# Performance work log

Hardware: AMD Instinct MI355X
Metric: run time of the kernel (lower is better)

Reference implementation:

```python
import jax, jax.numpy as jnp
import numpy as np

N = 50000          # nodes
E = 1600000        # edges
IN_C = 128
HID = 128
OUT_C = 1
NUM_LAYERS = 3     # extra conv2 applications
NUM_GRAPHS = 128


def setup_inputs() -> dict:
    key = jax.random.key(0)
    ks = jax.random.split(key, 10)
    x = jax.random.normal(ks[0], (N, IN_C), dtype=jnp.float32)
    edge_index = jax.random.randint(ks[1], (2, E), 0, N, dtype=jnp.int64)
    batch = jnp.sort(jax.random.randint(ks[2], (N,), 0, NUM_GRAPHS, dtype=jnp.int64))
    s1 = 1.0 / np.sqrt(IN_C)
    s2 = 1.0 / np.sqrt(HID)
    W1 = jax.random.uniform(ks[3], (IN_C, HID), jnp.float32, -s1, s1)
    b1 = jnp.zeros((HID,), jnp.float32)
    W2 = jax.random.uniform(ks[4], (HID, HID), jnp.float32, -s2, s2)
    b2 = jnp.zeros((HID,), jnp.float32)
    Wfc = jax.random.uniform(ks[5], (HID, OUT_C), jnp.float32, -s2, s2)
    bfc = jnp.zeros((OUT_C,), jnp.float32)
    return {"x": x, "edge_index": edge_index, "batch": batch,
            "W1": W1, "b1": b1, "W2": W2, "b2": b2, "Wfc": Wfc, "bfc": bfc}


def _gcn_conv(x, W, b, src, dst, dinv):
    # GCNConv: h = X W; out[i] = sum_{j->i} h[j]/sqrt(d_j d_i) + h[i]/d_i + b
    # (self-loops added, symmetric degree normalization, deg includes self-loop)
    h = x @ W                                   # [N, out]
    coef = dinv[src] * dinv[dst]                # [E]
    agg = jax.ops.segment_sum(h[src] * coef[:, None], dst, num_segments=N)
    agg = agg + h * (dinv * dinv)[:, None]      # self-loop contribution
    return agg + b


def reference(x, edge_index, batch, W1, b1, W2, b2, Wfc, bfc):
    src, dst = edge_index[0], edge_index[1]
    # degree of target nodes, +1 for self-loop
    deg = jax.ops.segment_sum(jnp.ones((E,), x.dtype), dst, num_segments=N) + 1.0
    dinv = jax.lax.rsqrt(deg)

    h = jax.nn.relu(_gcn_conv(x, W1, b1, src, dst, dinv))
    for _ in range(NUM_LAYERS):
        h = jax.nn.relu(_gcn_conv(h, W2, b2, src, dst, dinv))
    # dropout is identity here (eval / deterministic reference)

    # global_mean_pool over graphs in the batch
    sums = jax.ops.segment_sum(h, batch, num_segments=NUM_GRAPHS)
    counts = jax.ops.segment_sum(jnp.ones((N,), h.dtype), batch, num_segments=NUM_GRAPHS)
    pooled = sums / jnp.clip(counts, 1.0)[:, None]   # [G, HID]
    return pooled @ Wfc + bfc                        # [G, OUT_C]
```

## Files before the change

### kernel.cpp

```cpp
#include <hip/hip_runtime.h>
#include <hip/hip_bf16.h>


typedef float nfloat4 __attribute__((ext_vector_type(4)));

__global__ void count_deg_kernel(const int* __restrict__ dst, int* __restrict__ deg,
                                 int* __restrict__ pos, int E) {
    int i = blockIdx.x * blockDim.x + threadIdx.x;
    int e = i * 4;
    if (e + 3 < E) {
        int4 d = *(const int4*)(dst + e);
        int p0 = atomicAdd(&deg[d.x], 1);
        int p1 = atomicAdd(&deg[d.y], 1);
        int p2 = atomicAdd(&deg[d.z], 1);
        int p3 = atomicAdd(&deg[d.w], 1);
        *(int4*)(pos + e) = make_int4(p0, p1, p2, p3);
    } else {
        for (; e < E; e++) pos[e] = atomicAdd(&deg[dst[e]], 1);
    }
}

__global__ void scan_blocksum_kernel(const int* __restrict__ cnt, int* __restrict__ bsum,
                                     int n2) {
    __shared__ int red[256];
    int t = threadIdx.x;
    int i = blockIdx.x * 256 + t;
    red[t] = (i < n2) ? cnt[i] : 0;
    __syncthreads();
    for (int off = 128; off > 0; off >>= 1) {
        if (t < off) red[t] += red[t + off];
        __syncthreads();
    }
    if (t == 0) bsum[blockIdx.x] = red[0];
}

__global__ __launch_bounds__(1024) void scan_bsum_kernel(const int* __restrict__ bsum,
                                                         int* __restrict__ boff, int nb) {
    __shared__ int s[1024];
    int t = threadIdx.x;
    int v = (t < nb) ? bsum[t] : 0;
    s[t] = v;
    __syncthreads();
    for (int off = 1; off < 1024; off <<= 1) {
        int u = (t >= off) ? s[t - off] : 0;
        __syncthreads();
        s[t] += u;
        __syncthreads();
    }
    if (t < nb) boff[t] = s[t] - v;
}

__global__ void scan_final_kernel(const int* __restrict__ cnt, const int* __restrict__ boff,
                                  int* __restrict__ row, float* __restrict__ dinv,
                                  float* __restrict__ h0, float* __restrict__ h1,
                                  int n2, int ns) {
    __shared__ int s[256];
    int t = threadIdx.x;
    int b = blockIdx.x;
    int i = b * 256 + t;
    int v = (i < n2) ? cnt[i] : 0;
    s[t] = v;
    __syncthreads();
    for (int off = 1; off < 256; off <<= 1) {
        int u = (t >= off) ? s[t - off] : 0;
        __syncthreads();
        s[t] += u;
        __syncthreads();
    }
    int incl = s[t];
    int base = boff[b];
    if (i < n2) {
        row[i] = base + incl - v;
        dinv[i] = (float)(1.0 / sqrt((double)(v + 1)));
    }
    if (i == n2 - 1) row[n2] = base + incl;
    if (i < 128) {
        int p = i >> 5, c = i & 31;
        size_t off2 = (size_t)p * ns * 32 + (size_t)n2 * 32 + c;
        h0[off2] = 0.f;
        h1[off2] = 0.f;
    }
}

__global__ __launch_bounds__(256) void csr_fill_kernel(const int* __restrict__ src,
                                                       const int* __restrict__ dst,
                                                       const int* __restrict__ row,
                                                       const int* __restrict__ pos,
                                                       unsigned short* __restrict__ csr,
                                                       int E, int N) {
    int g  = blockIdx.x & 7;
    int gb = blockIdx.x >> 3;
    int group_blocks = gridDim.x >> 3;
    int R  = (N + 7) >> 3;
    int lo = g * R;
    int hi = lo + R; if (hi > N) hi = N;

    int tig    = gb * blockDim.x + threadIdx.x;
    int stride = group_blocks * blockDim.x;
    int nq = (E + 3) >> 2;

    for (int q = tig; q < nq; q += stride) {
        int e = q * 4;
        if (e + 3 < E) {
            int4 d = *(const int4*)(dst + e);
            if (d.x >= lo && d.x < hi) csr[row[d.x] + pos[e + 0]] = (unsigned short)src[e + 0];
            if (d.y >= lo && d.y < hi) csr[row[d.y] + pos[e + 1]] = (unsigned short)src[e + 1];
            if (d.z >= lo && d.z < hi) csr[row[d.z] + pos[e + 2]] = (unsigned short)src[e + 2];
            if (d.w >= lo && d.w < hi) csr[row[d.w] + pos[e + 3]] = (unsigned short)src[e + 3];
        } else {
            for (; e < E; e++) {
                int d = dst[e];
                if (d >= lo && d < hi) csr[row[d] + pos[e]] = (unsigned short)src[e];
            }
        }
    }
}

__global__ __launch_bounds__(256) void gemm_kernel(const float* __restrict__ A,
                                                   const float* __restrict__ W,
                                                   const float* __restrict__ dinv,
                                                   float* __restrict__ C, int n, int ns,
                                                   int a_blocked) {
    __shared__ float sW[2][16 * 128];
    __shared__ float sA[2][16 * 68];
    int t = threadIdx.x;
    int row0 = blockIdx.x * 64;

    int a_rowi = t >> 2;
    int a_q    = t & 3;
    int w_krow = t >> 4;
    int w_c    = (t & 15) * 8;

    auto a_src = [&](int kb) -> const float* {
        int rr = row0 + a_rowi; if (rr > n - 1) rr = n - 1;
        return a_blocked
            ? (A + ((size_t)(kb >> 1) * ns + rr) * 32 + (kb & 1) * 16 + a_q * 4)
            : (A + (size_t)rr * 128 + kb * 16 + a_q * 4);
    };

    {
        float4 av = *(const float4*)a_src(0);
        float4 w0 = *(const float4*)(W + (size_t)w_krow * 128 + w_c);
        float4 w1 = *(const float4*)(W + (size_t)w_krow * 128 + w_c + 4);
        sA[0][(a_q * 4 + 0) * 68 + a_rowi] = av.x;
        sA[0][(a_q * 4 + 1) * 68 + a_rowi] = av.y;
        sA[0][(a_q * 4 + 2) * 68 + a_rowi] = av.z;
        sA[0][(a_q * 4 + 3) * 68 + a_rowi] = av.w;
        *(float4*)(&sW[0][w_krow * 128 + w_c])     = w0;
        *(float4*)(&sW[0][w_krow * 128 + w_c + 4]) = w1;
    }
    __syncthreads();

    int rg = t >> 4;
    int c0 = (t & 15) * 4;

    float acc[4][8];
    #pragma unroll
    for (int j = 0; j < 4; j++)
        #pragma unroll
        for (int c = 0; c < 8; c++) acc[j][c] = 0.f;

    #pragma unroll 1
    for (int kb = 0; kb < 8; kb++) {
        float4 pa, pw0, pw1;
        if (kb < 7) {
            pa  = *(const float4*)a_src(kb + 1);
            pw0 = *(const float4*)(W + (size_t)((kb + 1) * 16 + w_krow) * 128 + w_c);
            pw1 = *(const float4*)(W + (size_t)((kb + 1) * 16 + w_krow) * 128 + w_c + 4);
        }

        const float* ab = sA[kb & 1];
        const float* wb = sW[kb & 1];
        #pragma unroll
        for (int k = 0; k < 16; k++) {
            float4 a4 = *(const float4*)(ab + k * 68 + rg * 4);
            float4 w0 = *(const float4*)(wb + k * 128 + c0);
            float4 w1 = *(const float4*)(wb + k * 128 + c0 + 64);
            #pragma unroll
            for (int j = 0; j < 4; j++) {
                float av = (j == 0) ? a4.x : (j == 1) ? a4.y : (j == 2) ? a4.z : a4.w;
                acc[j][0] = fmaf(av, w0.x, acc[j][0]);
                acc[j][1] = fmaf(av, w0.y, acc[j][1]);
                acc[j][2] = fmaf(av, w0.z, acc[j][2]);
                acc[j][3] = fmaf(av, w0.w, acc[j][3]);
                acc[j][4] = fmaf(av, w1.x, acc[j][4]);
                acc[j][5] = fmaf(av, w1.y, acc[j][5]);
                acc[j][6] = fmaf(av, w1.z, acc[j][6]);
                acc[j][7] = fmaf(av, w1.w, acc[j][7]);
            }
        }

        if (kb < 7) {
            int nb = (kb + 1) & 1;
            sA[nb][(a_q * 4 + 0) * 68 + a_rowi] = pa.x;
            sA[nb][(a_q * 4 + 1) * 68 + a_rowi] = pa.y;
            sA[nb][(a_q * 4 + 2) * 68 + a_rowi] = pa.z;
            sA[nb][(a_q * 4 + 3) * 68 + a_rowi] = pa.w;
            *(float4*)(&sW[nb][w_krow * 128 + w_c])     = pw0;
            *(float4*)(&sW[nb][w_krow * 128 + w_c + 4]) = pw1;
        }
        __syncthreads();
    }

    float* Cb0 = C + (size_t)(c0 >> 5) * ns * 32 + (c0 & 31);
    float* Cb1 = C + (size_t)((c0 + 64) >> 5) * ns * 32 + ((c0 + 64) & 31);
    #pragma unroll
    for (int j = 0; j < 4; j++) {
        int rr = row0 + rg * 4 + j;
        if (rr < n) {
            float dsc = dinv[rr];
            *(float4*)(Cb0 + (size_t)rr * 32) =
                make_float4(acc[j][0] * dsc, acc[j][1] * dsc,
                            acc[j][2] * dsc, acc[j][3] * dsc);
            *(float4*)(Cb1 + (size_t)rr * 32) =
                make_float4(acc[j][4] * dsc, acc[j][5] * dsc,
                            acc[j][6] * dsc, acc[j][7] * dsc);
        }
    }
}

__global__ __launch_bounds__(256) void agg_kernel(const float* __restrict__ h,
                                                  const int* __restrict__ row_ptr,
                                                  const unsigned short* __restrict__ csr,
                                                  const float* __restrict__ dinv,
                                                  const float* __restrict__ bias,
                                                  float* __restrict__ out,
                                                  int n, int ns) {
    int p = blockIdx.x & 3;
    int i = (blockIdx.x >> 2) * 32 + (threadIdx.x >> 3);
    int q = threadIdx.x & 7;
    bool valid = (i < n);
    int iv = valid ? i : 0;

    const float* slice  = h   + (size_t)p * ns * 32;
    float*       oslice = out + (size_t)p * ns * 32;

    int beg = row_ptr[iv];
    int end = valid ? row_ptr[iv + 1] : beg;
    int qoff = q << 2;

    float di = dinv[iv];
    float4 self = *(const float4*)(slice + ((size_t)iv << 5) + qoff);
    float4 b4   = *(const float4*)(bias + p * 32 + qoff);

    float4 acc = make_float4(0.f, 0.f, 0.f, 0.f);

    int e = beg;
    int s0 = (int)__builtin_nontemporal_load(csr + e);
    int s1 = (int)__builtin_nontemporal_load(csr + e + 1);
    int s2 = (int)__builtin_nontemporal_load(csr + e + 2);
    int s3 = (int)__builtin_nontemporal_load(csr + e + 3);
    int s4 = (int)__builtin_nontemporal_load(csr + e + 4);
    int s5 = (int)__builtin_nontemporal_load(csr + e + 5);
    int s6 = (int)__builtin_nontemporal_load(csr + e + 6);
    int s7 = (int)__builtin_nontemporal_load(csr + e + 7);

    while (__any(e < end)) {
        int en = e + 8;
        int t0 = (int)__builtin_nontemporal_load(csr + en);
        int t1 = (int)__builtin_nontemporal_load(csr + en + 1);
        int t2 = (int)__builtin_nontemporal_load(csr + en + 2);
        int t3 = (int)__builtin_nontemporal_load(csr + en + 3);
        int t4 = (int)__builtin_nontemporal_load(csr + en + 4);
        int t5 = (int)__builtin_nontemporal_load(csr + en + 5);
        int t6 = (int)__builtin_nontemporal_load(csr + en + 6);
        int t7 = (int)__builtin_nontemporal_load(csr + en + 7);

        int g0 = (e     < end) ? s0 : n;
        int g1 = (e + 1 < end) ? s1 : n;
        int g2 = (e + 2 < end) ? s2 : n;
        int g3 = (e + 3 < end) ? s3 : n;
        int g4 = (e + 4 < end) ? s4 : n;
        int g5 = (e + 5 < end) ? s5 : n;
        int g6 = (e + 6 < end) ? s6 : n;
        int g7 = (e + 7 < end) ? s7 : n;

        float4 v0 = *(const float4*)(slice + ((size_t)g0 << 5) + qoff);
        float4 v1 = *(const float4*)(slice + ((size_t)g1 << 5) + qoff);
        float4 v2 = *(const float4*)(slice + ((size_t)g2 << 5) + qoff);
        float4 v3 = *(const float4*)(slice + ((size_t)g3 << 5) + qoff);
        float4 v4 = *(const float4*)(slice + ((size_t)g4 << 5) + qoff);
        float4 v5 = *(const float4*)(slice + ((size_t)g5 << 5) + qoff);
        float4 v6 = *(const float4*)(slice + ((size_t)g6 << 5) + qoff);
        float4 v7 = *(const float4*)(slice + ((size_t)g7 << 5) + qoff);

        acc.x += v0.x; acc.y += v0.y; acc.z += v0.z; acc.w += v0.w;
        acc.x += v1.x; acc.y += v1.y; acc.z += v1.z; acc.w += v1.w;
        acc.x += v2.x; acc.y += v2.y; acc.z += v2.z; acc.w += v2.w;
        acc.x += v3.x; acc.y += v3.y; acc.z += v3.z; acc.w += v3.w;
        acc.x += v4.x; acc.y += v4.y; acc.z += v4.z; acc.w += v4.w;
        acc.x += v5.x; acc.y += v5.y; acc.z += v5.z; acc.w += v5.w;
        acc.x += v6.x; acc.y += v6.y; acc.z += v6.z; acc.w += v6.w;
        acc.x += v7.x; acc.y += v7.y; acc.z += v7.z; acc.w += v7.w;

        e = en;
        s0 = t0; s1 = t1; s2 = t2; s3 = t3;
        s4 = t4; s5 = t5; s6 = t6; s7 = t7;
    }

    if (valid) {
        nfloat4 o;
        o.x = fmaxf(fmaf(acc.x + self.x, di, b4.x), 0.f);
        o.y = fmaxf(fmaf(acc.y + self.y, di, b4.y), 0.f);
        o.z = fmaxf(fmaf(acc.z + self.z, di, b4.z), 0.f);
        o.w = fmaxf(fmaf(acc.w + self.w, di, b4.w), 0.f);
        __builtin_nontemporal_store(o, (nfloat4*)(oslice + ((size_t)i << 5) + qoff));
    }
}

__global__ __launch_bounds__(128) void pool_partial_kernel(const float* __restrict__ h,
                                                           const int* __restrict__ batch,
                                                           double* __restrict__ partials,
                                                           int n, int ns, int S) {
    int g = blockIdx.x / S;
    int s = blockIdx.x % S;
    int c = threadIdx.x;
    const float* hb = h + (size_t)(c >> 5) * ns * 32 + (c & 31);

    int lo = 0, hi = n;
    while (lo < hi) { int mid = (lo + hi) >> 1; if (batch[mid] < g) lo = mid + 1; else hi = mid; }
    int start = lo;
    lo = start; hi = n;
    while (lo < hi) { int mid = (lo + hi) >> 1; if (batch[mid] < g + 1) lo = mid + 1; else hi = mid; }
    int end = lo;

    int cnt = end - start;
    int per = (cnt + S - 1) / S;
    int rs = start + s * per;
    int re = rs + per; if (re > end) re = end;

    double a0 = 0.0, a1 = 0.0, a2 = 0.0, a3 = 0.0;
    int r = rs;
    for (; r + 4 <= re; r += 4) {
        a0 += (double)hb[(size_t)(r + 0) * 32];
        a1 += (double)hb[(size_t)(r + 1) * 32];
        a2 += (double)hb[(size_t)(r + 2) * 32];
        a3 += (double)hb[(size_t)(r + 3) * 32];
    }
    for (; r < re; r++) a0 += (double)hb[(size_t)r * 32];
    partials[(size_t)(g * S + s) * 128 + c] = (a0 + a1) + (a2 + a3);
}

__global__ __launch_bounds__(128) void pool_fc_final_kernel(const double* __restrict__ partials,
                                                            const int* __restrict__ batch,
                                                            const float* __restrict__ Wfc,
                                                            const float* __restrict__ bfc,
                                                            float* __restrict__ out,
                                                            int n, int S) {
    int g = blockIdx.x;
    int c = threadIdx.x;

    int lo = 0, hi = n;
    while (lo < hi) { int mid = (lo + hi) >> 1; if (batch[mid] < g) lo = mid + 1; else hi = mid; }
    int start = lo;
    lo = start; hi = n;
    while (lo < hi) { int mid = (lo + hi) >> 1; if (batch[mid] < g + 1) lo = mid + 1; else hi = mid; }
    int cnt = lo - start;

    double sum = 0.0;
    for (int s = 0; s < S; s++) sum += partials[(size_t)(g * S + s) * 128 + c];
    double mean = sum / (double)(cnt > 0 ? cnt : 1);
    double v = mean * (double)Wfc[c];

    __shared__ double red[128];
    red[c] = v;
    __syncthreads();
    for (int off = 64; off > 0; off >>= 1) {
        if (c < off) red[c] += red[c + off];
        __syncthreads();
    }
    if (c == 0) out[g] = (float)(red[0] + (double)bfc[0]);
}

extern "C" void kernel_launch(void* const* d_in, const int* in_sizes, int n_in,
                              void* d_out, int out_size, void* d_ws, size_t ws_size,
                              hipStream_t stream) {
    const float* x          = (const float*)d_in[0];
    const int*   edge_index = (const int*)d_in[1];
    const int*   batch      = (const int*)d_in[2];
    const float* W1  = (const float*)d_in[3];
    const float* b1  = (const float*)d_in[4];
    const float* W2  = (const float*)d_in[5];
    const float* b2  = (const float*)d_in[6];
    const float* Wfc = (const float*)d_in[7];
    const float* bfc = (const float*)d_in[8];
    float* out = (float*)d_out;

    const int N = in_sizes[2];
    const int E = in_sizes[1] / 2;
    const int G = out_size;
    const int NS = N + 1;

    const int* e_src = edge_index;
    const int* e_dst = edge_index + E;

    char* p = (char*)d_ws;
    auto alloc = [&](size_t bytes) {
        void* r = (void*)p;
        p += (bytes + 255) & ~(size_t)255;
        return r;
    };
    const int S = 8;
    const int NB = (N + 255) / 256;
    float*          h0        = (float*)alloc((size_t)NS * 128 * 4);
    float*          h1        = (float*)alloc((size_t)NS * 128 * 4);
    unsigned short* csr       = (unsigned short*)alloc(((size_t)E + 1024) * 2);
    int*            row       = (int*)  alloc((size_t)(N + 1) * 4);
    int*            deg       = (int*)  alloc((size_t)N * 4);
    int*            pos       = (int*)  alloc((size_t)(E + 4) * 4);
    int*            bsum      = (int*)  alloc((size_t)NB * 4);
    int*            boff      = (int*)  alloc((size_t)NB * 4);
    float*          dinv      = (float*)alloc((size_t)N * 4);
    double*         partials  = (double*)alloc((size_t)G * S * 128 * 8);
    (void)ws_size; (void)n_in;

    hipMemsetAsync(deg, 0, (size_t)N * 4, stream);

    int tb = 256;
    int e4 = (E + 3) / 4;
    count_deg_kernel<<<(e4 + tb - 1) / tb, tb, 0, stream>>>(e_dst, deg, pos, E);
    scan_blocksum_kernel<<<NB, 256, 0, stream>>>(deg, bsum, N);
    scan_bsum_kernel<<<1, 1024, 0, stream>>>(bsum, boff, NB);
    scan_final_kernel<<<NB, 256, 0, stream>>>(deg, boff, row, dinv, h0, h1, N, NS);
    csr_fill_kernel<<<1024, tb, 0, stream>>>(e_src, e_dst, row, pos, csr, E, N);

    int gemm_blocks = (N + 63) / 64;
    int agg_blocks  = 4 * ((N + 31) / 32);

    gemm_kernel<<<gemm_blocks, 256, 0, stream>>>(x, W1, dinv, h1, N, NS, 0);
    agg_kernel<<<agg_blocks, 256, 0, stream>>>(h1, row, csr, dinv, b1, h0, N, NS);

    for (int l = 0; l < 3; l++) {
        gemm_kernel<<<gemm_blocks, 256, 0, stream>>>(h0, W2, dinv, h1, N, NS, 1);
        agg_kernel<<<agg_blocks, 256, 0, stream>>>(h1, row, csr, dinv, b2, h0, N, NS);
    }

    pool_partial_kernel<<<G * S, 128, 0, stream>>>(h0, batch, partials, N, NS, S);
    pool_fc_final_kernel<<<G, 128, 0, stream>>>(partials, batch, Wfc, bfc, out, N, S);
}
```

Measured before the change: 653.9 us.

## Fuse CSR preprocessing kernels into one cooperative kernel with grid syncs

```diff
diff --git a/kernel.cpp b/kernel.cpp
--- a/kernel.cpp
+++ b/kernel.cpp
@@ -1,116 +1,117 @@
 #include <hip/hip_runtime.h>
 #include <hip/hip_bf16.h>
+#include <hip/hip_cooperative_groups.h>
+
+namespace cg = cooperative_groups;
 
 
 typedef float nfloat4 __attribute__((ext_vector_type(4)));
 
-__global__ void count_deg_kernel(const int* __restrict__ dst, int* __restrict__ deg,
-                                 int* __restrict__ pos, int E) {
-    int i = blockIdx.x * blockDim.x + threadIdx.x;
-    int e = i * 4;
-    if (e + 3 < E) {
-        int4 d = *(const int4*)(dst + e);
-        int p0 = atomicAdd(&deg[d.x], 1);
-        int p1 = atomicAdd(&deg[d.y], 1);
-        int p2 = atomicAdd(&deg[d.z], 1);
-        int p3 = atomicAdd(&deg[d.w], 1);
-        *(int4*)(pos + e) = make_int4(p0, p1, p2, p3);
-    } else {
-        for (; e < E; e++) pos[e] = atomicAdd(&deg[dst[e]], 1);
-    }
-}
-
-__global__ void scan_blocksum_kernel(const int* __restrict__ cnt, int* __restrict__ bsum,
-                                     int n2) {
-    __shared__ int red[256];
-    int t = threadIdx.x;
-    int i = blockIdx.x * 256 + t;
-    red[t] = (i < n2) ? cnt[i] : 0;
-    __syncthreads();
-    for (int off = 128; off > 0; off >>= 1) {
-        if (t < off) red[t] += red[t + off];
-        __syncthreads();
-    }
-    if (t == 0) bsum[blockIdx.x] = red[0];
-}
-
-__global__ __launch_bounds__(1024) void scan_bsum_kernel(const int* __restrict__ bsum,
-                                                         int* __restrict__ boff, int nb) {
-    __shared__ int s[1024];
-    int t = threadIdx.x;
-    int v = (t < nb) ? bsum[t] : 0;
-    s[t] = v;
-    __syncthreads();
-    for (int off = 1; off < 1024; off <<= 1) {
-        int u = (t >= off) ? s[t - off] : 0;
-        __syncthreads();
-        s[t] += u;
-        __syncthreads();
-    }
-    if (t < nb) boff[t] = s[t] - v;
-}
-
-__global__ void scan_final_kernel(const int* __restrict__ cnt, const int* __restrict__ boff,
-                                  int* __restrict__ row, float* __restrict__ dinv,
-                                  float* __restrict__ h0, float* __restrict__ h1,
-                                  int n2, int ns) {
+__global__ __launch_bounds__(256) void preproc_kernel(
+    const int* __restrict__ src, const int* __restrict__ dst,
+    int* __restrict__ deg, int* __restrict__ pos,
+    int* __restrict__ bsum, int* __restrict__ boff,
+    int* __restrict__ row, float* __restrict__ dinv,
+    float* __restrict__ h0, float* __restrict__ h1,
+    unsigned short* __restrict__ csr,
+    int E, int N, int ns)
+{
+    cg::grid_group grid = cg::this_grid();
     __shared__ int s[256];
-    int t = threadIdx.x;
-    int b = blockIdx.x;
-    int i = b * 256 + t;
-    int v = (i < n2) ? cnt[i] : 0;
-    s[t] = v;
-    __syncthreads();
-    for (int off = 1; off < 256; off <<= 1) {
-        int u = (t >= off) ? s[t - off] : 0;
-        __syncthreads();
-        s[t] += u;
-        __syncthreads();
-    }
-    int incl = s[t];
-    int base = boff[b];
-    if (i < n2) {
-        row[i] = base + incl - v;
-        dinv[i] = (float)(1.0 / sqrt((double)(v + 1)));
-    }
-    if (i == n2 - 1) row[n2] = base + incl;
-    if (i < 128) {
-        int p = i >> 5, c = i & 31;
-        size_t off2 = (size_t)p * ns * 32 + (size_t)n2 * 32 + c;
-        h0[off2] = 0.f;
-        h1[off2] = 0.f;
-    }
-}
-
-__global__ __launch_bounds__(256) void csr_fill_kernel(const int* __restrict__ src,
-                                                       const int* __restrict__ dst,
-                                                       const int* __restrict__ row,
-                                                       const int* __restrict__ pos,
-                                                       unsigned short* __restrict__ csr,
-                                                       int E, int N) {
-    int g  = blockIdx.x & 7;
-    int gb = blockIdx.x >> 3;
-    int group_blocks = gridDim.x >> 3;
-    int R  = (N + 7) >> 3;
-    int lo = g * R;
-    int hi = lo + R; if (hi > N) hi = N;
-
-    int tig    = gb * blockDim.x + threadIdx.x;
-    int stride = group_blocks * blockDim.x;
+    int t = threadIdx.x, b = blockIdx.x;
+    int gid = b * 256 + t;
+    int gsz = gridDim.x * 256;
+
+    for (int i = gid; i < N; i += gsz) deg[i] = 0;
+    grid.sync();
+
     int nq = (E + 3) >> 2;
-
-    for (int q = tig; q < nq; q += stride) {
+    for (int q = gid; q < nq; q += gsz) {
         int e = q * 4;
         if (e + 3 < E) {
             int4 d = *(const int4*)(dst + e);
-            if (d.x >= lo && d.x < hi) csr[row[d.x] + pos[e + 0]] = (unsigned short)src[e + 0];
-            if (d.y >= lo && d.y < hi) csr[row[d.y] + pos[e + 1]] = (unsigned short)src[e + 1];
-            if (d.z >= lo && d.z < hi) csr[row[d.z] + pos[e + 2]] = (unsigned short)src[e + 2];
-            if (d.w >= lo && d.w < hi) csr[row[d.w] + pos[e + 3]] = (unsigned short)src[e + 3];
+            int p0 = atomicAdd(&deg[d.x], 1);
+            int p1 = atomicAdd(&deg[d.y], 1);
+            int p2 = atomicAdd(&deg[d.z], 1);
+            int p3 = atomicAdd(&deg[d.w], 1);
+            *(int4*)(pos + e) = make_int4(p0, p1, p2, p3);
         } else {
-            for (; e < E; e++) {
-                int d = dst[e];
-                if (d >= lo && d < hi) csr[row[d] + pos[e]] = (unsigned short)src[e];
+            for (; e < E; e++) pos[e] = atomicAdd(&deg[dst[e]], 1);
+        }
+    }
+    grid.sync();
+
+    int NB = (N + 255) >> 8;
+    int v = 0, incl = 0;
+    if (b < NB) {
+        int i = b * 256 + t;
+        v = (i < N) ? deg[i] : 0;
+        s[t] = v;
+        __syncthreads();
+        for (int off = 1; off < 256; off <<= 1) {
+            int u = (t >= off) ? s[t - off] : 0;
+            __syncthreads();
+            s[t] += u;
+            __syncthreads();
+        }
+        incl = s[t];
+        if (t == 255) bsum[b] = incl;
+    }
+    grid.sync();
+
+    if (b == 0) {
+        int w = (t < NB) ? bsum[t] : 0;
+        s[t] = w;
+        __syncthreads();
+        for (int off = 1; off < 256; off <<= 1) {
+            int u = (t >= off) ? s[t - off] : 0;
+            __syncthreads();
+            s[t] += u;
+            __syncthreads();
+        }
+        if (t < NB) boff[t] = s[t] - w;
+    }
+    grid.sync();
+
+    if (b < NB) {
+        int base = boff[b];
+        int i = b * 256 + t;
+        if (i < N) {
+            row[i] = base + incl - v;
+            dinv[i] = (float)(1.0 / sqrt((double)(v + 1)));
+        }
+        if (i == N - 1) row[N] = base + incl;
+    }
+    if (gid < 128) {
+        int p = gid >> 5, c = gid & 31;
+        size_t off2 = (size_t)p * ns * 32 + (size_t)N * 32 + c;
+        h0[off2] = 0.f;
+        h1[off2] = 0.f;
+    }
+    grid.sync();
+
+    {
+        int g8 = b & 7;
+        int gb = b >> 3;
+        int group_blocks = gridDim.x >> 3;
+        int R = (N + 7) >> 3;
+        int lo = g8 * R;
+        int hi = lo + R; if (hi > N) hi = N;
+        int tig = gb * 256 + t;
+        int stride = group_blocks * 256;
+        for (int q = tig; q < nq; q += stride) {
+            int e = q * 4;
+            if (e + 3 < E) {
+                int4 d = *(const int4*)(dst + e);
+                if (d.x >= lo && d.x < hi) csr[row[d.x] + pos[e + 0]] = (unsigned short)src[e + 0];
+                if (d.y >= lo && d.y < hi) csr[row[d.y] + pos[e + 1]] = (unsigned short)src[e + 1];
+                if (d.z >= lo && d.z < hi) csr[row[d.z] + pos[e + 2]] = (unsigned short)src[e + 2];
+                if (d.w >= lo && d.w < hi) csr[row[d.w] + pos[e + 3]] = (unsigned short)src[e + 3];
+            } else {
+                for (; e < E; e++) {
+                    int d = dst[e];
+                    if (d >= lo && d < hi) csr[row[d] + pos[e]] = (unsigned short)src[e];
+                }
             }
         }
     }
@@ -414,15 +415,17 @@
     double*         partials  = (double*)alloc((size_t)G * S * 128 * 8);
     (void)ws_size; (void)n_in;
 
-    hipMemsetAsync(deg, 0, (size_t)N * 4, stream);
-
-    int tb = 256;
-    int e4 = (E + 3) / 4;
-    count_deg_kernel<<<(e4 + tb - 1) / tb, tb, 0, stream>>>(e_dst, deg, pos, E);
-    scan_blocksum_kernel<<<NB, 256, 0, stream>>>(deg, bsum, N);
-    scan_bsum_kernel<<<1, 1024, 0, stream>>>(bsum, boff, NB);
-    scan_final_kernel<<<NB, 256, 0, stream>>>(deg, boff, row, dinv, h0, h1, N, NS);
-    csr_fill_kernel<<<1024, tb, 0, stream>>>(e_src, e_dst, row, pos, csr, E, N);
+    {
+        int Ei = E, Ni = N, NSi = NS;
+        void* args[] = {
+            (void*)&e_src, (void*)&e_dst, (void*)&deg, (void*)&pos,
+            (void*)&bsum, (void*)&boff, (void*)&row, (void*)&dinv,
+            (void*)&h0, (void*)&h1, (void*)&csr,
+            (void*)&Ei, (void*)&Ni, (void*)&NSi
+        };
+        hipLaunchCooperativeKernel((void*)preproc_kernel, dim3(1024), dim3(256),
+                                   args, 0, stream);
+    }
 
     int gemm_blocks = (N + 63) / 64;
     int agg_blocks  = 4 * ((N + 31) / 32);
```

After: 1.123 ms. 1.72x slower.
